# Kernel tuning notes

Hardware: AMD Instinct MI355X
Metric: run time of the kernel (lower is better)

## Reference

```python
import jax, jax.numpy as jnp
import numpy as np

B, T_CACHE, N_STATE, N_HEAD = 128, 448, 1280, 20
HEAD_DIM = N_STATE // N_HEAD


def setup_inputs() -> dict:
    key = jax.random.key(0)
    ks = jax.random.split(key, 10)
    s = 1.0 / np.sqrt(N_STATE)
    return {
        "x": jax.random.normal(ks[0], (B, 1, N_STATE), jnp.float32),
        "k_cache": jax.random.normal(ks[1], (B, T_CACHE, N_STATE), jnp.float32),
        "v_cache": jax.random.normal(ks[2], (B, T_CACHE, N_STATE), jnp.float32),
        "mask": jnp.zeros((1, T_CACHE), jnp.float32),
        "Wq": jax.random.normal(ks[3], (N_STATE, N_STATE), jnp.float32) * s,
        "bq": jax.random.normal(ks[4], (N_STATE,), jnp.float32) * s,
        "Wk": jax.random.normal(ks[5], (N_STATE, N_STATE), jnp.float32) * s,
        "Wv": jax.random.normal(ks[6], (N_STATE, N_STATE), jnp.float32) * s,
        "bv": jax.random.normal(ks[7], (N_STATE,), jnp.float32) * s,
        "Wo": jax.random.normal(ks[8], (N_STATE, N_STATE), jnp.float32) * s,
        "bo": jax.random.normal(ks[9], (N_STATE,), jnp.float32) * s,
    }


def reference(x, k_cache, v_cache, mask, Wq, bq, Wk, Wv, bv, Wo, bo):
    b, q_len, n_state = x.shape  # q_len == 1 in loop (streaming) mode
    h, d = N_HEAD, n_state // N_HEAD

    # Q/K/V projections (Whisper: key has no bias)
    q = x @ Wq + bq                         # [B, 1, n_state]
    k = x @ Wk                              # [B, 1, n_state]
    v = x @ Wv + bv                         # [B, 1, n_state]

    # streaming KV-cache shift-and-append
    k_cache = jnp.concatenate([k_cache[:, 1:, :], k], axis=1)  # [B, T, n_state]
    v_cache = jnp.concatenate([v_cache[:, 1:, :], v], axis=1)

    t = k_cache.shape[1]
    scale = d ** (-0.25)
    qh = q.reshape(b, q_len, h, d).transpose(0, 2, 1, 3) * scale   # [B, H, q, d]
    kh = k_cache.reshape(b, t, h, d).transpose(0, 2, 3, 1) * scale  # [B, H, d, T]
    vh = v_cache.reshape(b, t, h, d).transpose(0, 2, 1, 3)          # [B, H, T, d]

    qk = jnp.matmul(qh, kh) + mask          # [B, H, q, T]
    qk = qk.astype(jnp.float32)
    w = jax.nn.softmax(qk, axis=-1).astype(qh.dtype)
    wv = jnp.matmul(w, vh)                  # [B, H, q, d]
    wv = wv.transpose(0, 2, 1, 3).reshape(b, q_len, n_state)

    out = wv @ Wo + bo                      # [B, q, n_state]
    return out, k_cache, v_cache
```

## Files before the change

kernel.cpp:

```cpp
#include <hip/hip_runtime.h>
#include <cstddef>

#define NSTATE 1280
#define TCACHE 448
#define NBATCH 128
#define NHEAD  20
#define HDIM   64
#define NT     8
#define RPC    (TCACHE / NT)

__device__ __forceinline__ void gemm_partial(const float* __restrict__ A,
                                             const float* __restrict__ B,
                                             float* __restrict__ C,
                                             int kb, int ke)
{
    __shared__ float As[32][64];
    __shared__ float Bs[32][32];
    const int tid = threadIdx.x;
    const int m0 = blockIdx.y * 64;
    const int n0 = blockIdx.x * 32;
    const int tr = tid >> 4;
    const int tc = tid & 15;
    float acc[4][2] = {{0.f,0.f},{0.f,0.f},{0.f,0.f},{0.f,0.f}};

    for (int k0 = kb; k0 < ke; k0 += 32) {
        #pragma unroll
        for (int j = 0; j < 2; ++j) {
            int chunk = tid * 2 + j;
            int row   = chunk >> 3;
            int kc    = (chunk & 7) << 2;
            float4 a = *(const float4*)(A + (size_t)(m0 + row) * NSTATE + k0 + kc);
            As[kc+0][row] = a.x; As[kc+1][row] = a.y;
            As[kc+2][row] = a.z; As[kc+3][row] = a.w;
        }
        {
            int row = tid >> 3;
            int nc  = (tid & 7) << 2;
            float4 b4 = *(const float4*)(B + (size_t)(k0 + row) * NSTATE + n0 + nc);
            *(float4*)&Bs[row][nc] = b4;
        }
        __syncthreads();
        #pragma unroll
        for (int kk = 0; kk < 32; ++kk) {
            float4 a = *(const float4*)&As[kk][tr << 2];
            float2 b = *(const float2*)&Bs[kk][tc << 1];
            acc[0][0] = fmaf(a.x, b.x, acc[0][0]); acc[0][1] = fmaf(a.x, b.y, acc[0][1]);
            acc[1][0] = fmaf(a.y, b.x, acc[1][0]); acc[1][1] = fmaf(a.y, b.y, acc[1][1]);
            acc[2][0] = fmaf(a.z, b.x, acc[2][0]); acc[2][1] = fmaf(a.z, b.y, acc[2][1]);
            acc[3][0] = fmaf(a.w, b.x, acc[3][0]); acc[3][1] = fmaf(a.w, b.y, acc[3][1]);
        }
        __syncthreads();
    }
    const int n = n0 + (tc << 1);
    #pragma unroll
    for (int i = 0; i < 4; ++i) {
        size_t m = (size_t)(m0 + (tr << 2) + i);
        C[m * NSTATE + n]     = acc[i][0];
        C[m * NSTATE + n + 1] = acc[i][1];
    }
}

__global__ void __launch_bounds__(256) proj_kernel(
    const float* __restrict__ x,
    const float* __restrict__ Wq, const float* __restrict__ Wk,
    const float* __restrict__ Wv, float* __restrict__ pp)
{
    const int z = blockIdx.z;
    const int mat = z >> 1, sp = z & 1;
    const float* B = (mat == 0) ? Wq : (mat == 1 ? Wk : Wv);
    gemm_partial(x, B, pp + (size_t)z * NBATCH * NSTATE, sp * 640, sp * 640 + 640);
}

__global__ void __launch_bounds__(256) proj_reduce_kernel(
    const float* __restrict__ pp, const float* __restrict__ bq,
    const float* __restrict__ bv, float* __restrict__ q_ws,
    float* __restrict__ kout, float* __restrict__ vout)
{
    const int mat = blockIdx.y;
    const size_t idx = ((size_t)blockIdx.x * 256 + threadIdx.x) * 4;
    const int b = (int)(idx / NSTATE), col = (int)(idx % NSTATE);
    const float* p0 = pp + (size_t)(mat * 2) * NBATCH * NSTATE + idx;
    const float* p1 = p0 + (size_t)NBATCH * NSTATE;
    float4 a = *(const float4*)p0, c = *(const float4*)p1;
    float4 v = make_float4(a.x + c.x, a.y + c.y, a.z + c.z, a.w + c.w);
    if (mat == 0) {
        float4 bb = *(const float4*)(bq + col);
        v.x = (v.x + bb.x) * 0.125f; v.y = (v.y + bb.y) * 0.125f;
        v.z = (v.z + bb.z) * 0.125f; v.w = (v.w + bb.w) * 0.125f;
        *(float4*)(q_ws + idx) = v;
    } else if (mat == 1) {
        *(float4*)(kout + ((size_t)b * TCACHE + TCACHE - 1) * NSTATE + col) = v;
    } else {
        float4 bb = *(const float4*)(bv + col);
        v.x += bb.x; v.y += bb.y; v.z += bb.z; v.w += bb.w;
        *(float4*)(vout + ((size_t)b * TCACHE + TCACHE - 1) * NSTATE + col) = v;
    }
}

__global__ void __launch_bounds__(320) scorek_kernel(
    const float* __restrict__ kin, const float* __restrict__ q_ws,
    const float* __restrict__ mask, float* __restrict__ kout,
    float* __restrict__ sc_ws)
{
    const int tc = blockIdx.x, b = blockIdx.y;
    const int tid = threadIdx.x;
    const int h = tid >> 4;
    const int col = tid << 2;
    const size_t base = (size_t)b * TCACHE * NSTATE;
    const float4 q4 = *(const float4*)(q_ws + (size_t)b * NSTATE + col);
    const int t0 = tc * RPC;
    #pragma unroll 4
    for (int r = 0; r < RPC; ++r) {
        const int t = t0 + r;
        const float* src = (t < TCACHE - 1)
            ? kin  + base + (size_t)(t + 1) * NSTATE + col
            : kout + base + (size_t)t * NSTATE + col;
        float4 kv = *(const float4*)src;
        if (t < TCACHE - 1)
            *(float4*)(kout + base + (size_t)t * NSTATE + col) = kv;
        float p = kv.x * q4.x + kv.y * q4.y + kv.z * q4.z + kv.w * q4.w;
        p += __shfl_xor(p, 1); p += __shfl_xor(p, 2);
        p += __shfl_xor(p, 4); p += __shfl_xor(p, 8);
        if ((tid & 15) == 0)
            sc_ws[((size_t)b * NHEAD + h) * TCACHE + t] = p + mask[t];
    }
}

__global__ void __launch_bounds__(256) softmax_kernel(float* __restrict__ sc)
{
    const int bh = blockIdx.x * 4 + (threadIdx.x >> 6);
    const int lane = threadIdx.x & 63;
    float* row = sc + (size_t)bh * TCACHE;
    float v[7];
    float m = -1e30f;
    #pragma unroll
    for (int i = 0; i < 7; ++i) { v[i] = row[i * 64 + lane]; m = fmaxf(m, v[i]); }
    #pragma unroll
    for (int d = 1; d <= 32; d <<= 1) m = fmaxf(m, __shfl_xor(m, d));
    float s = 0.f;
    #pragma unroll
    for (int i = 0; i < 7; ++i) { v[i] = __expf(v[i] - m); s += v[i]; }
    #pragma unroll
    for (int d = 1; d <= 32; d <<= 1) s += __shfl_xor(s, d);
    const float inv = 1.0f / s;
    #pragma unroll
    for (int i = 0; i < 7; ++i) row[i * 64 + lane] = v[i] * inv;
}

__global__ void __launch_bounds__(320) pvv_kernel(
    const float* __restrict__ vin, const float* __restrict__ w_ws,
    float* __restrict__ vout, float* __restrict__ wvp)
{
    const int tc = blockIdx.x, b = blockIdx.y;
    const int tid = threadIdx.x;
    const int h = tid >> 4;
    const int col = tid << 2;
    const int t0 = tc * RPC;
    __shared__ float wl[NHEAD * RPC];
    for (int i = tid; i < NHEAD * RPC; i += 320) {
        int hh = i / RPC, rr = i - hh * RPC;
        wl[i] = w_ws[((size_t)b * NHEAD + hh) * TCACHE + t0 + rr];
    }
    __syncthreads();
    const size_t base = (size_t)b * TCACHE * NSTATE;
    float4 acc = make_float4(0.f, 0.f, 0.f, 0.f);
    #pragma unroll 4
    for (int r = 0; r < RPC; ++r) {
        const int t = t0 + r;
        const float* src = (t < TCACHE - 1)
            ? vin  + base + (size_t)(t + 1) * NSTATE + col
            : vout + base + (size_t)t * NSTATE + col;
        float4 vv = *(const float4*)src;
        if (t < TCACHE - 1)
            *(float4*)(vout + base + (size_t)t * NSTATE + col) = vv;
        const float w = wl[h * RPC + r];
        acc.x = fmaf(w, vv.x, acc.x); acc.y = fmaf(w, vv.y, acc.y);
        acc.z = fmaf(w, vv.z, acc.z); acc.w = fmaf(w, vv.w, acc.w);
    }
    *(float4*)(wvp + ((size_t)b * NT + tc) * NSTATE + col) = acc;
}

__global__ void __launch_bounds__(256) wv_reduce_kernel(
    const float* __restrict__ wvp, float* __restrict__ wv_ws)
{
    const size_t idx = ((size_t)blockIdx.x * 256 + threadIdx.x) * 4;
    const int b = (int)(idx / NSTATE), col = (int)(idx % NSTATE);
    float4 s = make_float4(0.f, 0.f, 0.f, 0.f);
    #pragma unroll
    for (int c = 0; c < NT; ++c) {
        float4 a = *(const float4*)(wvp + ((size_t)b * NT + c) * NSTATE + col);
        s.x += a.x; s.y += a.y; s.z += a.z; s.w += a.w;
    }
    *(float4*)(wv_ws + idx) = s;
}

__global__ void __launch_bounds__(256) outproj_kernel(
    const float* __restrict__ wv, const float* __restrict__ Wo,
    float* __restrict__ po)
{
    const int sp = blockIdx.z;
    gemm_partial(wv, Wo, po + (size_t)sp * NBATCH * NSTATE, sp * 320, sp * 320 + 320);
}

__global__ void __launch_bounds__(256) out_reduce_kernel(
    const float* __restrict__ po, const float* __restrict__ bo,
    float* __restrict__ out)
{
    const size_t idx = ((size_t)blockIdx.x * 256 + threadIdx.x) * 4;
    const int col = (int)(idx % NSTATE);
    float4 s = *(const float4*)(bo + col);
    #pragma unroll
    for (int c = 0; c < 4; ++c) {
        float4 a = *(const float4*)(po + (size_t)c * NBATCH * NSTATE + idx);
        s.x += a.x; s.y += a.y; s.z += a.z; s.w += a.w;
    }
    *(float4*)(out + idx) = s;
}

extern "C" void kernel_launch(void* const* d_in, const int* in_sizes, int n_in,
                              void* d_out, int out_size, void* d_ws, size_t ws_size,
                              hipStream_t stream)
{
    const float* x       = (const float*)d_in[0];
    const float* k_cache = (const float*)d_in[1];
    const float* v_cache = (const float*)d_in[2];
    const float* mask    = (const float*)d_in[3];
    const float* Wq      = (const float*)d_in[4];
    const float* bq      = (const float*)d_in[5];
    const float* Wk      = (const float*)d_in[6];
    const float* Wv      = (const float*)d_in[7];
    const float* bv      = (const float*)d_in[8];
    const float* Wo      = (const float*)d_in[9];
    const float* bo      = (const float*)d_in[10];

    float* out  = (float*)d_out;
    float* kout = out + (size_t)NBATCH * NSTATE;
    float* vout = kout + (size_t)NBATCH * TCACHE * NSTATE;

    float* ws     = (float*)d_ws;
    float* q_ws   = ws;
    float* sc_ws  = q_ws  + (size_t)NBATCH * NSTATE;
    float* wvp_ws = sc_ws + (size_t)NBATCH * NHEAD * TCACHE;
    float* pp_ws  = wvp_ws + (size_t)NBATCH * NT * NSTATE;
    float* po_ws  = pp_ws + (size_t)6 * NBATCH * NSTATE;
    float* wv_ws  = po_ws + (size_t)4 * NBATCH * NSTATE;

    proj_kernel<<<dim3(40, 2, 6), 256, 0, stream>>>(x, Wq, Wk, Wv, pp_ws);
    proj_reduce_kernel<<<dim3(160, 3), 256, 0, stream>>>(pp_ws, bq, bv,
                                                         q_ws, kout, vout);
    scorek_kernel<<<dim3(NT, NBATCH), 320, 0, stream>>>(k_cache, q_ws, mask,
                                                        kout, sc_ws);
    softmax_kernel<<<dim3(NBATCH * NHEAD / 4), 256, 0, stream>>>(sc_ws);
    pvv_kernel<<<dim3(NT, NBATCH), 320, 0, stream>>>(v_cache, sc_ws, vout, wvp_ws);
    wv_reduce_kernel<<<dim3(160), 256, 0, stream>>>(wvp_ws, wv_ws);
    outproj_kernel<<<dim3(40, 2, 4), 256, 0, stream>>>(wv_ws, Wo, po_ws);
    out_reduce_kernel<<<dim3(160), 256, 0, stream>>>(po_ws, bo, out);
}
```

Baseline: 318.2 us.

## Fuse projection reduce, softmax into neighbors; use nontemporal cache copies

```diff
diff --git a/kernel.cpp b/kernel.cpp
--- a/kernel.cpp
+++ b/kernel.cpp
@@ -9,10 +9,13 @@
 #define NT     8
 #define RPC    (TCACHE / NT)
 
-__device__ __forceinline__ void gemm_partial(const float* __restrict__ A,
-                                             const float* __restrict__ B,
-                                             float* __restrict__ C,
-                                             int kb, int ke)
+typedef float f4 __attribute__((ext_vector_type(4)));
+
+__device__ __forceinline__ void gemm_body(const float* __restrict__ A,
+                                          const float* __restrict__ B,
+                                          const float* __restrict__ bias,
+                                          float* __restrict__ C, size_t ldc,
+                                          int kb, int ke, float scale)
 {
     __shared__ float As[32][64];
     __shared__ float Bs[32][32];
@@ -52,48 +55,32 @@
         __syncthreads();
     }
     const int n = n0 + (tc << 1);
+    const float b0 = bias ? bias[n]   : 0.f;
+    const float b1 = bias ? bias[n+1] : 0.f;
     #pragma unroll
     for (int i = 0; i < 4; ++i) {
         size_t m = (size_t)(m0 + (tr << 2) + i);
-        C[m * NSTATE + n]     = acc[i][0];
-        C[m * NSTATE + n + 1] = acc[i][1];
-    }
-}
-
-__global__ void __launch_bounds__(256) proj_kernel(
+        C[m * ldc + n]     = (acc[i][0] + b0) * scale;
+        C[m * ldc + n + 1] = (acc[i][1] + b1) * scale;
+    }
+}
+
+__global__ void __launch_bounds__(256) proj_qkv_kernel(
     const float* __restrict__ x,
-    const float* __restrict__ Wq, const float* __restrict__ Wk,
-    const float* __restrict__ Wv, float* __restrict__ pp)
+    const float* __restrict__ Wq, const float* __restrict__ bq,
+    const float* __restrict__ Wk,
+    const float* __restrict__ Wv, const float* __restrict__ bv,
+    float* __restrict__ q_ws, float* __restrict__ kout, float* __restrict__ vout)
 {
     const int z = blockIdx.z;
-    const int mat = z >> 1, sp = z & 1;
-    const float* B = (mat == 0) ? Wq : (mat == 1 ? Wk : Wv);
-    gemm_partial(x, B, pp + (size_t)z * NBATCH * NSTATE, sp * 640, sp * 640 + 640);
-}
-
-__global__ void __launch_bounds__(256) proj_reduce_kernel(
-    const float* __restrict__ pp, const float* __restrict__ bq,
-    const float* __restrict__ bv, float* __restrict__ q_ws,
-    float* __restrict__ kout, float* __restrict__ vout)
-{
-    const int mat = blockIdx.y;
-    const size_t idx = ((size_t)blockIdx.x * 256 + threadIdx.x) * 4;
-    const int b = (int)(idx / NSTATE), col = (int)(idx % NSTATE);
-    const float* p0 = pp + (size_t)(mat * 2) * NBATCH * NSTATE + idx;
-    const float* p1 = p0 + (size_t)NBATCH * NSTATE;
-    float4 a = *(const float4*)p0, c = *(const float4*)p1;
-    float4 v = make_float4(a.x + c.x, a.y + c.y, a.z + c.z, a.w + c.w);
-    if (mat == 0) {
-        float4 bb = *(const float4*)(bq + col);
-        v.x = (v.x + bb.x) * 0.125f; v.y = (v.y + bb.y) * 0.125f;
-        v.z = (v.z + bb.z) * 0.125f; v.w = (v.w + bb.w) * 0.125f;
-        *(float4*)(q_ws + idx) = v;
-    } else if (mat == 1) {
-        *(float4*)(kout + ((size_t)b * TCACHE + TCACHE - 1) * NSTATE + col) = v;
+    if (z == 0) {
+        gemm_body(x, Wq, bq, q_ws, NSTATE, 0, NSTATE, 0.125f);
+    } else if (z == 1) {
+        gemm_body(x, Wk, nullptr, kout + (size_t)(TCACHE-1) * NSTATE,
+                  (size_t)TCACHE * NSTATE, 0, NSTATE, 1.0f);
     } else {
-        float4 bb = *(const float4*)(bv + col);
-        v.x += bb.x; v.y += bb.y; v.z += bb.z; v.w += bb.w;
-        *(float4*)(vout + ((size_t)b * TCACHE + TCACHE - 1) * NSTATE + col) = v;
+        gemm_body(x, Wv, bv, vout + (size_t)(TCACHE-1) * NSTATE,
+                  (size_t)TCACHE * NSTATE, 0, NSTATE, 1.0f);
     }
 }
 
@@ -109,75 +96,81 @@
     const size_t base = (size_t)b * TCACHE * NSTATE;
     const float4 q4 = *(const float4*)(q_ws + (size_t)b * NSTATE + col);
     const int t0 = tc * RPC;
+    const int nrows = (tc == NT - 1) ? RPC - 1 : RPC;
+    const float* src0 = kin + base + (size_t)(t0 + 1) * NSTATE + col;
+    float* dst0 = kout + base + (size_t)t0 * NSTATE + col;
+    float* scrow = sc_ws + ((size_t)b * NHEAD + h) * TCACHE + t0;
+
     #pragma unroll 4
-    for (int r = 0; r < RPC; ++r) {
-        const int t = t0 + r;
-        const float* src = (t < TCACHE - 1)
-            ? kin  + base + (size_t)(t + 1) * NSTATE + col
-            : kout + base + (size_t)t * NSTATE + col;
-        float4 kv = *(const float4*)src;
-        if (t < TCACHE - 1)
-            *(float4*)(kout + base + (size_t)t * NSTATE + col) = kv;
-        float p = kv.x * q4.x + kv.y * q4.y + kv.z * q4.z + kv.w * q4.w;
+    for (int r = 0; r < nrows; ++r) {
+        f4 kv = __builtin_nontemporal_load((const f4*)(src0 + (size_t)r * NSTATE));
+        __builtin_nontemporal_store(kv, (f4*)(dst0 + (size_t)r * NSTATE));
+        float p = kv[0]*q4.x + kv[1]*q4.y + kv[2]*q4.z + kv[3]*q4.w;
         p += __shfl_xor(p, 1); p += __shfl_xor(p, 2);
         p += __shfl_xor(p, 4); p += __shfl_xor(p, 8);
-        if ((tid & 15) == 0)
-            sc_ws[((size_t)b * NHEAD + h) * TCACHE + t] = p + mask[t];
-    }
-}
-
-__global__ void __launch_bounds__(256) softmax_kernel(float* __restrict__ sc)
-{
-    const int bh = blockIdx.x * 4 + (threadIdx.x >> 6);
-    const int lane = threadIdx.x & 63;
-    float* row = sc + (size_t)bh * TCACHE;
-    float v[7];
-    float m = -1e30f;
-    #pragma unroll
-    for (int i = 0; i < 7; ++i) { v[i] = row[i * 64 + lane]; m = fmaxf(m, v[i]); }
-    #pragma unroll
-    for (int d = 1; d <= 32; d <<= 1) m = fmaxf(m, __shfl_xor(m, d));
-    float s = 0.f;
-    #pragma unroll
-    for (int i = 0; i < 7; ++i) { v[i] = __expf(v[i] - m); s += v[i]; }
-    #pragma unroll
-    for (int d = 1; d <= 32; d <<= 1) s += __shfl_xor(s, d);
-    const float inv = 1.0f / s;
-    #pragma unroll
-    for (int i = 0; i < 7; ++i) row[i * 64 + lane] = v[i] * inv;
+        if ((tid & 15) == 0) scrow[r] = p + mask[t0 + r];
+    }
+    if (tc == NT - 1) {
+        const f4 kv = *(const f4*)(kout + base + (size_t)(TCACHE-1) * NSTATE + col);
+        float p = kv[0]*q4.x + kv[1]*q4.y + kv[2]*q4.z + kv[3]*q4.w;
+        p += __shfl_xor(p, 1); p += __shfl_xor(p, 2);
+        p += __shfl_xor(p, 4); p += __shfl_xor(p, 8);
+        if ((tid & 15) == 0) scrow[RPC - 1] = p + mask[TCACHE - 1];
+    }
 }
 
 __global__ void __launch_bounds__(320) pvv_kernel(
-    const float* __restrict__ vin, const float* __restrict__ w_ws,
+    const float* __restrict__ vin, const float* __restrict__ sc_ws,
     float* __restrict__ vout, float* __restrict__ wvp)
 {
     const int tc = blockIdx.x, b = blockIdx.y;
     const int tid = threadIdx.x;
-    const int h = tid >> 4;
+    const int h = tid >> 4, l = tid & 15;
     const int col = tid << 2;
     const int t0 = tc * RPC;
     __shared__ float wl[NHEAD * RPC];
-    for (int i = tid; i < NHEAD * RPC; i += 320) {
-        int hh = i / RPC, rr = i - hh * RPC;
-        wl[i] = w_ws[((size_t)b * NHEAD + hh) * TCACHE + t0 + rr];
+
+    const float* row = sc_ws + ((size_t)b * NHEAD + h) * TCACHE;
+    float v[28];
+    float m = -1e30f;
+    #pragma unroll
+    for (int j = 0; j < 28; ++j) { v[j] = row[l + 16*j]; m = fmaxf(m, v[j]); }
+    #pragma unroll
+    for (int d = 1; d <= 8; d <<= 1) m = fmaxf(m, __shfl_xor(m, d));
+    float s = 0.f;
+    #pragma unroll
+    for (int j = 0; j < 28; ++j) s += __expf(v[j] - m);
+    #pragma unroll
+    for (int d = 1; d <= 8; d <<= 1) s += __shfl_xor(s, d);
+    const float inv = 1.0f / s;
+    #pragma unroll
+    for (int j = 0; j < 4; ++j) {
+        int r = l + 16*j;
+        if (r < RPC) wl[h * RPC + r] = __expf(row[t0 + r] - m) * inv;
     }
     __syncthreads();
+
     const size_t base = (size_t)b * TCACHE * NSTATE;
-    float4 acc = make_float4(0.f, 0.f, 0.f, 0.f);
+    const int nrows = (tc == NT - 1) ? RPC - 1 : RPC;
+    const float* src0 = vin + base + (size_t)(t0 + 1) * NSTATE + col;
+    float* dst0 = vout + base + (size_t)t0 * NSTATE + col;
+    float ax = 0.f, ay = 0.f, az = 0.f, aw = 0.f;
     #pragma unroll 4
-    for (int r = 0; r < RPC; ++r) {
-        const int t = t0 + r;
-        const float* src = (t < TCACHE - 1)
-            ? vin  + base + (size_t)(t + 1) * NSTATE + col
-            : vout + base + (size_t)t * NSTATE + col;
-        float4 vv = *(const float4*)src;
-        if (t < TCACHE - 1)
-            *(float4*)(vout + base + (size_t)t * NSTATE + col) = vv;
+    for (int r = 0; r < nrows; ++r) {
+        f4 vv = __builtin_nontemporal_load((const f4*)(src0 + (size_t)r * NSTATE));
+        __builtin_nontemporal_store(vv, (f4*)(dst0 + (size_t)r * NSTATE));
         const float w = wl[h * RPC + r];
-        acc.x = fmaf(w, vv.x, acc.x); acc.y = fmaf(w, vv.y, acc.y);
-        acc.z = fmaf(w, vv.z, acc.z); acc.w = fmaf(w, vv.w, acc.w);
-    }
-    *(float4*)(wvp + ((size_t)b * NT + tc) * NSTATE + col) = acc;
+        ax = fmaf(w, vv[0], ax); ay = fmaf(w, vv[1], ay);
+        az = fmaf(w, vv[2], az); aw = fmaf(w, vv[3], aw);
+    }
+    if (tc == NT - 1) {
+        const f4 vv = *(const f4*)(vout + base + (size_t)(TCACHE-1) * NSTATE + col);
+        const float w = wl[h * RPC + RPC - 1];
+        ax = fmaf(w, vv[0], ax); ay = fmaf(w, vv[1], ay);
+        az = fmaf(w, vv[2], az); aw = fmaf(w, vv[3], aw);
+    }
+    *(float4*)(wvp + ((size_t)b * NT + tc) * NSTATE + col) =
+        make_float4(ax, ay, az, aw);
 }
 
 __global__ void __launch_bounds__(256) wv_reduce_kernel(
@@ -199,7 +192,8 @@
     float* __restrict__ po)
 {
     const int sp = blockIdx.z;
-    gemm_partial(wv, Wo, po + (size_t)sp * NBATCH * NSTATE, sp * 320, sp * 320 + 320);
+    gemm_body(wv, Wo, nullptr, po + (size_t)sp * NBATCH * NSTATE,
+              NSTATE, sp * 320, sp * 320 + 320, 1.0f);
 }
 
 __global__ void __launch_bounds__(256) out_reduce_kernel(
@@ -241,16 +235,13 @@
     float* q_ws   = ws;
     float* sc_ws  = q_ws  + (size_t)NBATCH * NSTATE;
     float* wvp_ws = sc_ws + (size_t)NBATCH * NHEAD * TCACHE;
-    float* pp_ws  = wvp_ws + (size_t)NBATCH * NT * NSTATE;
-    float* po_ws  = pp_ws + (size_t)6 * NBATCH * NSTATE;
+    float* po_ws  = wvp_ws + (size_t)NBATCH * NT * NSTATE;
     float* wv_ws  = po_ws + (size_t)4 * NBATCH * NSTATE;
 
-    proj_kernel<<<dim3(40, 2, 6), 256, 0, stream>>>(x, Wq, Wk, Wv, pp_ws);
-    proj_reduce_kernel<<<dim3(160, 3), 256, 0, stream>>>(pp_ws, bq, bv,
-                                                         q_ws, kout, vout);
+    proj_qkv_kernel<<<dim3(40, 2, 3), 256, 0, stream>>>(x, Wq, bq, Wk, Wv, bv,
+                                                        q_ws, kout, vout);
     scorek_kernel<<<dim3(NT, NBATCH), 320, 0, stream>>>(k_cache, q_ws, mask,
                                                         kout, sc_ws);
-    softmax_kernel<<<dim3(NBATCH * NHEAD / 4), 256, 0, stream>>>(sc_ws);
     pvv_kernel<<<dim3(NT, NBATCH), 320, 0, stream>>>(v_cache, sc_ws, vout, wvp_ws);
     wv_reduce_kernel<<<dim3(160), 256, 0, stream>>>(wvp_ws, wv_ws);
     outproj_kernel<<<dim3(40, 2, 4), 256, 0, stream>>>(wv_ws, Wo, po_ws);
```

Result: no change. 317.6 us (-0.2%).
